# Kernel optimization log

Hardware: AMD Instinct MI355X
Metric: run time of the kernel (lower is better)

The kernel has to match this reference:

```python
import jax, jax.numpy as jnp
import numpy as np

EPS = 1e-5
K = 20  # n. neighbors


def _lrelu(x):
    return jnp.where(x >= 0, x, 0.2 * x)


def _bn(x, gamma, beta):
    # training-mode batchnorm over all axes except channel axis 1
    axes = tuple(i for i in range(x.ndim) if i != 1)
    m = jnp.mean(x, axis=axes, keepdims=True)
    v = jnp.var(x, axis=axes, keepdims=True)
    shape = [1, x.shape[1]] + [1] * (x.ndim - 2)
    return (x - m) * jax.lax.rsqrt(v + EPS) * gamma.reshape(shape) + beta.reshape(shape)


def _knn(x, k):
    # x: (B, C, N) -> idx (B, N, k) of nearest neighbors (largest negative sq dist)
    xx = jnp.sum(x * x, axis=1)                      # (B, N)
    inner = jnp.einsum('bcn,bcm->bnm', x, x)          # (B, N, N)
    dist = -xx[:, :, None] + 2.0 * inner - xx[:, None, :]
    _, idx = jax.lax.top_k(dist, k)
    return idx


def _graph_feature(x, k):
    # x: (B, C, N) -> edge features (B, 2C, N, k)
    B = x.shape[0]
    idx = _knn(x, k)                                  # (B, N, k)
    xt = jnp.transpose(x, (0, 2, 1))                  # (B, N, C)
    nbr = xt[jnp.arange(B)[:, None, None], idx]       # (B, N, k, C)
    ctr = xt[:, :, None, :]                           # (B, N, 1, C)
    edge = jnp.concatenate([nbr - ctr, jnp.broadcast_to(ctr, nbr.shape)], axis=-1)
    return jnp.transpose(edge, (0, 3, 1, 2))          # (B, 2C, N, k)


def _conv1d(W, x):
    return jnp.einsum('oc,bcn->bon', W, x)


def _conv2d(W, x):
    return jnp.einsum('oc,bcnk->bonk', W, x)


def setup_inputs() -> dict:
    key = jax.random.key(0)
    ks = jax.random.split(key, 10)
    w = lambda k, s: jax.random.normal(k, s, jnp.float32) * 0.05
    d = {
        'x': jax.random.normal(ks[0], (4, 3, 4096), jnp.float32),
        'W1': w(ks[1], (64, 3)),
        'W2': w(ks[2], (64, 128)),
        'W3': w(ks[3], (64, 128)),
        'W4': w(ks[4], (512, 64)),
        'W5': w(ks[5], (512, 704)),
        'W6': w(ks[6], (256, 512)),
        'W7': w(ks[7], (128, 256)),
        'W8': w(ks[8], (2, 128)),
        'bias8': jnp.zeros((2,), jnp.float32),
    }
    bn_ch = [64, 64, 64, 512, 512, 256, 128]
    for i, c in enumerate(bn_ch, start=1):
        d[f'gamma{i}'] = jnp.ones((c,), jnp.float32)
        d[f'beta{i}'] = jnp.zeros((c,), jnp.float32)
    return d


def reference(x, W1, W2, W3, W4, W5, W6, W7, W8, bias8,
              gamma1, beta1, gamma2, beta2, gamma3, beta3, gamma4, beta4,
              gamma5, beta5, gamma6, beta6, gamma7, beta7):
    N = x.shape[2]
    x1 = _lrelu(_bn(_conv1d(W1, x), gamma1, beta1))                 # (B,64,N)
    e2 = _graph_feature(x1, K)                                      # (B,128,N,k)
    x2 = _lrelu(_bn(_conv2d(W2, e2), gamma2, beta2)).max(axis=-1)   # (B,64,N)
    e3 = _graph_feature(x2, K)
    x3 = _lrelu(_bn(_conv2d(W3, e3), gamma3, beta3)).max(axis=-1)   # (B,64,N)
    x6 = _lrelu(_bn(_conv1d(W4, x3), gamma4, beta4))                # (B,512,N)
    x6 = jnp.broadcast_to(x6.max(axis=-1, keepdims=True), (x6.shape[0], x6.shape[1], N))
    x7 = jnp.concatenate([x1, x2, x3, x6], axis=1)                  # (B,704,N)
    x7 = _lrelu(_bn(_conv1d(W5, x7), gamma5, beta5))
    x7 = _lrelu(_bn(_conv1d(W6, x7), gamma6, beta6))
    x7 = _lrelu(_bn(_conv1d(W7, x7), gamma7, beta7))
    return _conv1d(W8, x7) + bias8[None, :, None]                   # (B,2,N)
```

## Files before the change

kernel.cpp:

```cpp
#include <hip/hip_runtime.h>
#include <math.h>

#define NN 4096
#define BB 4
#define NPT (NN*BB)
#define KK 20
#define EPSB 1e-5f

#define AS_STRIDE 132
#define WS_STRIDE 68
#define SKEW(c) ((((((c)>>2)&7))<<2) + (((c)>>5)*28))

__device__ __forceinline__ float lrelu(float x){ return x >= 0.f ? x : 0.2f*x; }

__device__ __forceinline__ unsigned fkey(float x){
  unsigned u = __float_as_uint(x);
  return u ^ (unsigned)(((int)u >> 31) | 0x80000000);
}

__global__ void conv1_kernel(const float* __restrict__ x, const float* __restrict__ W1,
                             float* __restrict__ xcat){
  __shared__ float Wl[192];
  int tid = threadIdx.x;
  if (tid < 192) Wl[tid] = W1[tid];
  __syncthreads();
  int p = blockIdx.x*4 + (tid >> 6);
  int o = tid & 63;
  int b = p >> 12, n = p & 4095;
  const float* xb = x + (size_t)b*3*NN + n;
  float acc = Wl[o*3+0]*xb[0] + Wl[o*3+1]*xb[NN] + Wl[o*3+2]*xb[2*NN];
  xcat[(size_t)p*192 + o] = acc;
}

__global__ void stats_pm_kernel(const float* __restrict__ buf, int stride, int ofs,
                                float* __restrict__ psum, float* __restrict__ psumsq, int C){
  int tid = threadIdx.x;
  int lane = tid & 63, g = tid >> 6;
  int o = blockIdx.x*64 + lane;
  int p0 = blockIdx.y*256 + g*64;
  float s = 0.f, ss = 0.f;
  for (int i = 0; i < 64; ++i){
    float v = buf[(size_t)(p0+i)*stride + ofs + o];
    s += v; ss += v*v;
  }
  __shared__ float rs[4][64], rss[4][64];
  rs[g][lane] = s; rss[g][lane] = ss;
  __syncthreads();
  if (g == 0){
    s  = rs[0][lane]+rs[1][lane]+rs[2][lane]+rs[3][lane];
    ss = rss[0][lane]+rss[1][lane]+rss[2][lane]+rss[3][lane];
    psum[(size_t)blockIdx.y*C + o] = s;
    psumsq[(size_t)blockIdx.y*C + o] = ss;
  }
}

__global__ void bn_finalize_kernel(const float* __restrict__ psum, const float* __restrict__ psumsq,
                                   int nparts,
                                   const float* __restrict__ gamma, const float* __restrict__ beta,
                                   float* __restrict__ scale, float* __restrict__ shift,
                                   float invcnt, int C){
  int o = threadIdx.x + blockIdx.x*blockDim.x;
  if (o >= C) return;
  float s = 0.f, ss = 0.f;
  for (int i = 0; i < nparts; ++i){
    s  += psum[(size_t)i*C + o];
    ss += psumsq[(size_t)i*C + o];
  }
  float m = s*invcnt;
  float v = ss*invcnt - m*m;
  v = fmaxf(v, 0.f);
  float sc = gamma[o] * rsqrtf(v + EPSB);
  scale[o] = sc;
  shift[o] = beta[o] - m*sc;
}

__global__ void apply_bn_kernel(float* __restrict__ buf, int stride, int ofs, int log2C,
                                const float* __restrict__ scale, const float* __restrict__ shift){
  int i = blockIdx.x*256 + threadIdx.x;
  int o = i & ((1<<log2C)-1);
  int p = i >> log2C;
  size_t a = (size_t)p*stride + ofs + o;
  float e = buf[a]*scale[o] + shift[o];
  buf[a] = lrelu(e);
}

__global__ void xx_kernel(const float* __restrict__ xcat, int stride, int ofs,
                          float* __restrict__ xx){
  int p = blockIdx.x*256 + threadIdx.x;
  const float4* r = (const float4*)(xcat + (size_t)p*stride + ofs);
  float s = 0.f;
  #pragma unroll
  for (int i = 0; i < 16; ++i){ float4 v = r[i]; s += v.x*v.x + v.y*v.y + v.z*v.z + v.w*v.w; }
  xx[p] = s;
}

__global__ void __launch_bounds__(256, 2)
dist_kernel(const float* __restrict__ xcat, int ofs,
            const float* __restrict__ xx, float* __restrict__ dist,
            unsigned* __restrict__ gmaxp, int b){
  int bx = blockIdx.x, by = blockIdx.y;
  if (by > bx) return;
  __shared__ float As[32*AS_STRIDE + 64];
  __shared__ float Bs[32*AS_STRIDE + 64];
  int tid = threadIdx.x;
  int n0 = by*128, m0 = bx*128;
  const float* base = xcat + (size_t)b*NN*192 + ofs;
  int pA = (tid >> 4)*4, oB = (tid & 15)*4;
  int cgrp = (tid & 7)*4;
  float acc[8][8] = {};
  for (int h = 0; h < 2; ++h){
    int cb = h*32;
    float4 vin[4], vw[4];
    #pragma unroll
    for (int j = 0; j < 4; ++j){
      int row = (tid + 256*j) >> 3;
      vin[j] = *(const float4*)(base + (size_t)(n0+row)*192 + cb + cgrp);
      vw[j]  = *(const float4*)(base + (size_t)(m0+row)*192 + cb + cgrp);
    }
    if (h) __syncthreads();
    #pragma unroll
    for (int j = 0; j < 4; ++j){
      int row = (tid + 256*j) >> 3, c4 = cgrp;
      float4 v = vin[j];
      As[(c4+0)*AS_STRIDE+SKEW(c4+0)+row]=v.x; As[(c4+1)*AS_STRIDE+SKEW(c4+1)+row]=v.y;
      As[(c4+2)*AS_STRIDE+SKEW(c4+2)+row]=v.z; As[(c4+3)*AS_STRIDE+SKEW(c4+3)+row]=v.w;
      float4 w = vw[j];
      Bs[(c4+0)*AS_STRIDE+SKEW(c4+0)+row]=w.x; Bs[(c4+1)*AS_STRIDE+SKEW(c4+1)+row]=w.y;
      Bs[(c4+2)*AS_STRIDE+SKEW(c4+2)+row]=w.z; Bs[(c4+3)*AS_STRIDE+SKEW(c4+3)+row]=w.w;
    }
    __syncthreads();
    for (int c = 0; c < 32; ++c){
      const float* arow = &As[c*AS_STRIDE + SKEW(c)];
      const float* brow = &Bs[c*AS_STRIDE + SKEW(c)];
      float4 a0 = *(const float4*)&arow[pA];
      float4 a1 = *(const float4*)&arow[pA + 64];
      float4 b0 = *(const float4*)&brow[oB];
      float4 b1 = *(const float4*)&brow[oB + 64];
      float av[8] = {a0.x,a0.y,a0.z,a0.w,a1.x,a1.y,a1.z,a1.w};
      float bv[8] = {b0.x,b0.y,b0.z,b0.w,b1.x,b1.y,b1.z,b1.w};
      #pragma unroll
      for (int i = 0; i < 8; ++i)
        #pragma unroll
        for (int j = 0; j < 8; ++j)
          acc[i][j] += av[i]*bv[j];
    }
  }
  float xmv[8], xnv[8];
  #pragma unroll
  for (int j = 0; j < 4; ++j){
    xmv[j]   = xx[b*NN + m0 + oB + j];
    xmv[4+j] = xx[b*NN + m0 + 64 + oB + j];
    xnv[j]   = xx[b*NN + n0 + pA + j];
    xnv[4+j] = xx[b*NN + n0 + 64 + pA + j];
  }
  #pragma unroll
  for (int h = 0; h < 2; ++h){
    #pragma unroll
    for (int i = 0; i < 4; ++i){
      int row = n0 + h*64 + pA + i;
      float xn = xnv[h*4 + i];
      int ai = h*4 + i;
      float4 w0, w1;
      w0.x = 2.f*acc[ai][0] - xn - xmv[0]; w0.y = 2.f*acc[ai][1] - xn - xmv[1];
      w0.z = 2.f*acc[ai][2] - xn - xmv[2]; w0.w = 2.f*acc[ai][3] - xn - xmv[3];
      w1.x = 2.f*acc[ai][4] - xn - xmv[4]; w1.y = 2.f*acc[ai][5] - xn - xmv[5];
      w1.z = 2.f*acc[ai][6] - xn - xmv[6]; w1.w = 2.f*acc[ai][7] - xn - xmv[7];
      float* drow = dist + (size_t)row*NN + m0;
      *(float4*)(drow + oB) = w0;
      *(float4*)(drow + 64 + oB) = w1;
      unsigned gm = fkey(w0.x), t;
      t = fkey(w0.y); if (t > gm) gm = t;
      t = fkey(w0.z); if (t > gm) gm = t;
      t = fkey(w0.w); if (t > gm) gm = t;
      t = fkey(w1.x); if (t > gm) gm = t;
      t = fkey(w1.y); if (t > gm) gm = t;
      t = fkey(w1.z); if (t > gm) gm = t;
      t = fkey(w1.w); if (t > gm) gm = t;
      gmaxp[(size_t)row*512 + (bx<<4) + (oB>>2)] = gm;
    }
  }
  if (bx != by){
    #pragma unroll
    for (int jh = 0; jh < 2; ++jh){
      #pragma unroll
      for (int jj = 0; jj < 4; ++jj){
        int j = jh*4 + jj;
        float xm = xmv[j];
        float4 lo, hi;
        lo.x = 2.f*acc[0][j] - xm - xnv[0];
        lo.y = 2.f*acc[1][j] - xm - xnv[1];
        lo.z = 2.f*acc[2][j] - xm - xnv[2];
        lo.w = 2.f*acc[3][j] - xm - xnv[3];
        hi.x = 2.f*acc[4][j] - xm - xnv[4];
        hi.y = 2.f*acc[5][j] - xm - xnv[5];
        hi.z = 2.f*acc[6][j] - xm - xnv[6];
        hi.w = 2.f*acc[7][j] - xm - xnv[7];
        int mrow = m0 + jh*64 + oB + jj;
        float* drow = dist + (size_t)mrow*NN + n0;
        *(float4*)(drow + pA) = lo;
        *(float4*)(drow + 64 + pA) = hi;
        unsigned gm = fkey(lo.x), t;
        t = fkey(lo.y); if (t > gm) gm = t;
        t = fkey(lo.z); if (t > gm) gm = t;
        t = fkey(lo.w); if (t > gm) gm = t;
        t = fkey(hi.x); if (t > gm) gm = t;
        t = fkey(hi.y); if (t > gm) gm = t;
        t = fkey(hi.z); if (t > gm) gm = t;
        t = fkey(hi.w); if (t > gm) gm = t;
        gmaxp[(size_t)mrow*512 + (by<<4) + (pA>>2)] = gm;
      }
    }
  }
}

__global__ void __launch_bounds__(256)
topk_kernel(const float* __restrict__ dist, const unsigned* __restrict__ gmax,
            int* __restrict__ idxout){
  __shared__ unsigned lv[4][256], li[4][256];
  __shared__ unsigned lcnt[4];
  int wv = threadIdx.x >> 6, lane = threadIdx.x & 63;
  int n = blockIdx.x*4 + wv;
  const unsigned* grow = gmax + (size_t)n*512;
  unsigned g[8];
  #pragma unroll
  for (int j = 0; j < 8; ++j) g[j] = grow[j*64 + lane];
  if (lane == 0) lcnt[wv] = 0u;
  unsigned prefix = 0u, act = 0xFFu; int need = KK; int tot = 512;
  for (int b = 31; b >= 16; --b){
    unsigned m = 0u;
    #pragma unroll
    for (int j = 0; j < 8; ++j) m |= ((g[j] >> b) & 1u) << j;
    unsigned c = (unsigned)__popc(m & act);
    #pragma unroll
    for (int s = 1; s < 64; s <<= 1) c += __shfl_xor(c, s);
    if ((int)c >= need){ act &= m; prefix |= (1u << b); tot = (int)c; }
    else { need -= (int)c; act &= ~m; tot -= (int)c; }
    if (KK - need + tot <= 44) break;
  }
  unsigned T = prefix;
  const float* drow = dist + (size_t)n*NN;
  #pragma unroll
  for (int j = 0; j < 8; ++j){
    if (g[j] >= T){
      int gid = j*64 + lane;
      int cbase = ((gid >> 4) << 7) + ((gid & 15) << 2);
      float4 v0 = *(const float4*)(drow + cbase);
      float4 v1 = *(const float4*)(drow + cbase + 64);
      unsigned k0=fkey(v0.x),k1=fkey(v0.y),k2=fkey(v0.z),k3=fkey(v0.w);
      unsigned k4=fkey(v1.x),k5=fkey(v1.y),k6=fkey(v1.z),k7=fkey(v1.w);
      int q = (k0>=T)+(k1>=T)+(k2>=T)+(k3>=T)+(k4>=T)+(k5>=T)+(k6>=T)+(k7>=T);
      unsigned pos = atomicAdd(&lcnt[wv], (unsigned)q);
      #define PUTC(kx,cofs) if (kx >= T){ if (pos < 256u){ lv[wv][pos]=kx; li[wv][pos]=(unsigned)(cbase+(cofs)); } pos++; }
      PUTC(k0,0) PUTC(k1,1) PUTC(k2,2) PUTC(k3,3)
      PUTC(k4,64) PUTC(k5,65) PUTC(k6,66) PUTC(k7,67)
      #undef PUTC
    }
  }
  unsigned C = lcnt[wv];
  int* orow = idxout + (size_t)n*KK;
  if (C <= 64u){
    unsigned kv = 0u, ki = 0xFFFFFFFFu;
    if (lane < (int)C){ kv = lv[wv][lane]; ki = li[wv][lane]; }
    #pragma unroll
    for (int k = 2; k <= 64; k <<= 1){
      #pragma unroll
      for (int j2 = k >> 1; j2 > 0; j2 >>= 1){
        unsigned ov = __shfl_xor(kv, j2);
        unsigned oi = __shfl_xor(ki, j2);
        bool iLower = ((lane & j2) == 0);
        bool dirDesc = ((lane & k) == 0);
        bool mineGr = (kv > ov) || (kv == ov && ki < oi);
        bool keep = dirDesc ? (iLower ? mineGr : !mineGr)
                            : (iLower ? !mineGr : mineGr);
        kv = keep ? kv : ov;
        ki = keep ? ki : oi;
      }
    }
    if (lane < KK) orow[lane] = (int)ki;
  } else {
    unsigned rv[KK], ri[KK];
    #pragma unroll
    for (int q = 0; q < KK; ++q){ rv[q]=0u; ri[q]=0xFFFFFFFFu; }
    #pragma unroll
    for (int j = 0; j < 8; ++j){
      if (g[j] >= T){
        int gid = j*64 + lane;
        int cbase = ((gid >> 4) << 7) + ((gid & 15) << 2);
        float4 v0 = *(const float4*)(drow + cbase);
        float4 v1 = *(const float4*)(drow + cbase + 64);
        float f0[8] = {v0.x,v0.y,v0.z,v0.w,v1.x,v1.y,v1.z,v1.w};
        #pragma unroll
        for (int t = 0; t < 8; ++t){
          unsigned u = fkey(f0[t]);
          unsigned ix = (unsigned)(cbase + ((t < 4) ? t : (60 + t)));
          bool beat = (u > rv[KK-1]) || (u == rv[KK-1] && ix < ri[KK-1]);
          if (u >= T && beat){
            unsigned pv = u, pi = ix;
            #pragma unroll
            for (int p = 0; p < KK; ++p){
              bool keep2 = (rv[p] > pv) || (rv[p] == pv && ri[p] < pi);
              unsigned nv = keep2 ? rv[p] : pv;
              unsigned ni = keep2 ? ri[p] : pi;
              pv = keep2 ? pv : rv[p];
              pi = keep2 ? pi : ri[p];
              rv[p] = nv; ri[p] = ni;
            }
          }
        }
      }
    }
    for (int q = 0; q < KK; ++q){
      unsigned bv = rv[0], bi = ri[0];
      #pragma unroll
      for (int s = 1; s < 64; s <<= 1){
        unsigned ov = __shfl_xor(bv, s);
        unsigned oi = __shfl_xor(bi, s);
        bool take = (ov > bv) || (ov == bv && oi < bi);
        bv = take ? ov : bv;
        bi = take ? oi : bi;
      }
      if (rv[0] == bv && ri[0] == bi){
        #pragma unroll
        for (int p = 0; p < KK-1; ++p){ rv[p] = rv[p+1]; ri[p] = ri[p+1]; }
        rv[KK-1] = 0u; ri[KK-1] = 0xFFFFFFFFu;
      }
      if (lane == 0) orow[q] = (int)bi;
    }
  }
}

__global__ void ut_kernel(const float* __restrict__ xcat, int ofs, const float* __restrict__ W,
                          float* __restrict__ U, float* __restrict__ T){
  __shared__ float Wl[64*129];
  int tid = threadIdx.x;
  for (int i = tid; i < 64*128; i += 256){
    int o = i >> 7, c = i & 127;
    Wl[o*129 + c] = W[i];
  }
  __syncthreads();
  int g = tid >> 6, lane = tid & 63;
  int p = blockIdx.x*4 + g;
  float xv = xcat[(size_t)p*192 + ofs + lane];
  const float* wr = Wl + lane*129;
  float u = 0.f, t = 0.f;
  for (int c = 0; c < 64; ++c){
    float xc = __shfl(xv, c);
    float wa = wr[c], wb = wr[64+c];
    u += wa*xc;
    t += (wb - wa)*xc;
  }
  U[(size_t)p*64 + lane] = u;
  T[(size_t)p*64 + lane] = t;
}

__global__ void gather_kernel(const float* __restrict__ U, const float* __restrict__ T,
                              const int* __restrict__ idx,
                              float* __restrict__ psum, float* __restrict__ psumsq,
                              float* __restrict__ vmax, float* __restrict__ vmin){
  int tid = threadIdx.x;
  int g = tid >> 6, lane = tid & 63;
  int p0 = blockIdx.x*64 + g*16;
  float s = 0.f, ss = 0.f;
  for (int pi = 0; pi < 16; ++pi){
    int p = p0 + pi;
    int base = (p >> 12) << 12;
    float t = T[(size_t)p*64 + lane];
    const int* ir = idx + (size_t)p*KK;
    float mx = -INFINITY, mn = INFINITY;
    for (int k = 0; k < KK; ++k){
      int j = ir[k];
      float v = U[(size_t)(base + j)*64 + lane] + t;
      s += v; ss += v*v;
      mx = fmaxf(mx, v); mn = fminf(mn, v);
    }
    vmax[(size_t)p*64 + lane] = mx;
    vmin[(size_t)p*64 + lane] = mn;
  }
  __shared__ float rs[4][64], rss[4][64];
  rs[g][lane] = s; rss[g][lane] = ss;
  __syncthreads();
  if (g == 0){
    s  = rs[0][lane]+rs[1][lane]+rs[2][lane]+rs[3][lane];
    ss = rss[0][lane]+rss[1][lane]+rss[2][lane]+rss[3][lane];
    psum[(size_t)blockIdx.x*64 + lane] = s;
    psumsq[(size_t)blockIdx.x*64 + lane] = ss;
  }
}

__global__ void gapply_kernel(const float* __restrict__ vmax, const float* __restrict__ vmin,
                              const float* __restrict__ scale, const float* __restrict__ shift,
                              float* __restrict__ xcat, int ofs){
  int i = blockIdx.x*256 + threadIdx.x;
  int p = i >> 6, o = i & 63;
  float s = scale[o];
  float v = (s >= 0.f) ? vmax[i] : vmin[i];
  xcat[(size_t)p*192 + ofs + o] = lrelu(s*v + shift[o]);
}

__global__ void __launch_bounds__(256, 2)
mm_kernel(const float* __restrict__ in, int inStride, int inOfs,
          const float* __restrict__ W, int wStride,
          float* __restrict__ out, int outStride,
          const float* __restrict__ bias, int O, int I,
          const float* __restrict__ bnScale, const float* __restrict__ bnShift){
  __shared__ float As[32*AS_STRIDE + 64];
  __shared__ float Ws[32*WS_STRIDE + 64];
  int tid = threadIdx.x;
  int p0 = blockIdx.x*128, o0 = blockIdx.y*64;
  int psub = (tid >> 4)*8, osub = (tid & 15)*4;
  int cgrp = (tid & 7)*4;
  float acc[8][4] = {};
  for (int cc = 0; cc < I; cc += 32){
    float4 sc4 = make_float4(1.f,1.f,1.f,1.f), sh4 = make_float4(0.f,0.f,0.f,0.f);
    if (bnScale){
      sc4 = *(const float4*)(bnScale + cc + cgrp);
      sh4 = *(const float4*)(bnShift + cc + cgrp);
    }
    float4 vin[4], vw[2];
    #pragma unroll
    for (int j = 0; j < 4; ++j){
      int row = (tid + 256*j) >> 3;
      vin[j] = *(const float4*)(in + (size_t)(p0+row)*inStride + inOfs + cc + cgrp);
    }
    #pragma unroll
    for (int j = 0; j < 2; ++j){
      int row = (tid + 256*j) >> 3;
      vw[j] = *(const float4*)(W + (size_t)(o0+row)*wStride + cc + cgrp);
    }
    if (cc) __syncthreads();
    #pragma unroll
    for (int j = 0; j < 4; ++j){
      int row = (tid + 256*j) >> 3, c4 = cgrp;
      float4 v = vin[j];
      if (bnScale){
        v.x = lrelu(v.x*sc4.x + sh4.x); v.y = lrelu(v.y*sc4.y + sh4.y);
        v.z = lrelu(v.z*sc4.z + sh4.z); v.w = lrelu(v.w*sc4.w + sh4.w);
      }
      As[(c4+0)*AS_STRIDE+SKEW(c4+0)+row]=v.x; As[(c4+1)*AS_STRIDE+SKEW(c4+1)+row]=v.y;
      As[(c4+2)*AS_STRIDE+SKEW(c4+2)+row]=v.z; As[(c4+3)*AS_STRIDE+SKEW(c4+3)+row]=v.w;
    }
    #pragma unroll
    for (int j = 0; j < 2; ++j){
      int row = (tid + 256*j) >> 3, c4 = cgrp;
      float4 v = vw[j];
      Ws[(c4+0)*WS_STRIDE+SKEW(c4+0)+row]=v.x; Ws[(c4+1)*WS_STRIDE+SKEW(c4+1)+row]=v.y;
      Ws[(c4+2)*WS_STRIDE+SKEW(c4+2)+row]=v.z; Ws[(c4+3)*WS_STRIDE+SKEW(c4+3)+row]=v.w;
    }
    __syncthreads();
    for (int c = 0; c < 32; ++c){
      const float* arow = &As[c*AS_STRIDE + SKEW(c)];
      const float* brow = &Ws[c*WS_STRIDE + SKEW(c)];
      float4 a0 = *(const float4*)&arow[psub];
      float4 a1 = *(const float4*)&arow[psub + 4];
      float4 bb = *(const float4*)&brow[osub];
      float av[8] = {a0.x,a0.y,a0.z,a0.w,a1.x,a1.y,a1.z,a1.w};
      float bv[4] = {bb.x,bb.y,bb.z,bb.w};
      #pragma unroll
      for (int i = 0; i < 8; ++i)
        #pragma unroll
        for (int j = 0; j < 4; ++j)
          acc[i][j] += av[i]*bv[j];
    }
  }
  int bIdx = p0 >> 12;
  float bb0=0.f, bb1=0.f, bb2=0.f, bb3=0.f;
  if (bias){
    bb0 = bias[bIdx*O + o0 + osub + 0];
    bb1 = bias[bIdx*O + o0 + osub + 1];
    bb2 = bias[bIdx*O + o0 + osub + 2];
    bb3 = bias[bIdx*O + o0 + osub + 3];
  }
  #pragma unroll
  for (int i = 0; i < 8; ++i){
    float4 w;
    w.x = acc[i][0]+bb0; w.y = acc[i][1]+bb1; w.z = acc[i][2]+bb2; w.w = acc[i][3]+bb3;
    *(float4*)(out + (size_t)(p0+psub+i)*outStride + o0 + osub) = w;
  }
}

__global__ void __launch_bounds__(256, 2)
mm64_kernel(const float* __restrict__ in, int inStride, int inOfs,
            const float* __restrict__ W, int wStride,
            float* __restrict__ out, int outStride,
            int O, int I,
            const float* __restrict__ bnScale, const float* __restrict__ bnShift){
  __shared__ float As[32*WS_STRIDE + 64];
  __shared__ float Ws[32*WS_STRIDE + 64];
  int tid = threadIdx.x;
  int p0 = blockIdx.x*64, o0 = blockIdx.y*64;
  int psub = (tid >> 4)*4, osub = (tid & 15)*4;
  int cgrp = (tid & 7)*4;
  float acc[4][4] = {};
  for (int cc = 0; cc < I; cc += 32){
    float4 sc4 = make_float4(1.f,1.f,1.f,1.f), sh4 = make_float4(0.f,0.f,0.f,0.f);
    if (bnScale){
      sc4 = *(const float4*)(bnScale + cc + cgrp);
      sh4 = *(const float4*)(bnShift + cc + cgrp);
    }
    float4 vin[2], vw[2];
    #pragma unroll
    for (int j = 0; j < 2; ++j){
      int row = (tid + 256*j) >> 3;
      vin[j] = *(const float4*)(in + (size_t)(p0+row)*inStride + inOfs + cc + cgrp);
      vw[j]  = *(const float4*)(W + (size_t)(o0+row)*wStride + cc + cgrp);
    }
    if (cc) __syncthreads();
    #pragma unroll
    for (int j = 0; j < 2; ++j){
      int row = (tid + 256*j) >> 3, c4 = cgrp;
      float4 v = vin[j];
      if (bnScale){
        v.x = lrelu(v.x*sc4.x + sh4.x); v.y = lrelu(v.y*sc4.y + sh4.y);
        v.z = lrelu(v.z*sc4.z + sh4.z); v.w = lrelu(v.w*sc4.w + sh4.w);
      }
      As[(c4+0)*WS_STRIDE+SKEW(c4+0)+row]=v.x; As[(c4+1)*WS_STRIDE+SKEW(c4+1)+row]=v.y;
      As[(c4+2)*WS_STRIDE+SKEW(c4+2)+row]=v.z; As[(c4+3)*WS_STRIDE+SKEW(c4+3)+row]=v.w;
      float4 w = vw[j];
      Ws[(c4+0)*WS_STRIDE+SKEW(c4+0)+row]=w.x; Ws[(c4+1)*WS_STRIDE+SKEW(c4+1)+row]=w.y;
      Ws[(c4+2)*WS_STRIDE+SKEW(c4+2)+row]=w.z; Ws[(c4+3)*WS_STRIDE+SKEW(c4+3)+row]=w.w;
    }
    __syncthreads();
    for (int c = 0; c < 32; ++c){
      const float* arow = &As[c*WS_STRIDE + SKEW(c)];
      const float* brow = &Ws[c*WS_STRIDE + SKEW(c)];
      float4 a0 = *(const float4*)&arow[psub];
      float4 bb = *(const float4*)&brow[osub];
      float av[4] = {a0.x,a0.y,a0.z,a0.w};
      float bv[4] = {bb.x,bb.y,bb.z,bb.w};
      #pragma unroll
      for (int i = 0; i < 4; ++i)
        #pragma unroll
        for (int j = 0; j < 4; ++j)
          acc[i][j] += av[i]*bv[j];
    }
  }
  #pragma unroll
  for (int i = 0; i < 4; ++i){
    float4 w;
    w.x = acc[i][0]; w.y = acc[i][1]; w.z = acc[i][2]; w.w = acc[i][3];
    *(float4*)(out + (size_t)(p0+psub+i)*outStride + o0 + osub) = w;
  }
}

__global__ void __launch_bounds__(256, 2)
conv4stats_kernel(const float* __restrict__ xcat, const float* __restrict__ W4,
                  float* __restrict__ psum, float* __restrict__ psumsq,
                  float* __restrict__ pmax, float* __restrict__ pmin){
  __shared__ float As[32*AS_STRIDE + 64];
  __shared__ float Ws[32*AS_STRIDE + 64];
  int tid = threadIdx.x;
  int p0 = blockIdx.x*128, o0 = blockIdx.y*128;
  int pA = (tid >> 4)*4, oB = (tid & 15)*4;
  int cgrp = (tid & 7)*4;
  float acc[8][8] = {};
  for (int h = 0; h < 2; ++h){
    int cb = h*32;
    float4 vin[4], vw[4];
    #pragma unroll
    for (int j = 0; j < 4; ++j){
      int row = (tid + 256*j) >> 3;
      vin[j] = *(const float4*)(xcat + (size_t)(p0+row)*192 + 128 + cb + cgrp);
      vw[j]  = *(const float4*)(W4 + (size_t)(o0+row)*64 + cb + cgrp);
    }
    if (h) __syncthreads();
    #pragma unroll
    for (int j = 0; j < 4; ++j){
      int row = (tid + 256*j) >> 3, c4 = cgrp;
      float4 v = vin[j];
      As[(c4+0)*AS_STRIDE+SKEW(c4+0)+row]=v.x; As[(c4+1)*AS_STRIDE+SKEW(c4+1)+row]=v.y;
      As[(c4+2)*AS_STRIDE+SKEW(c4+2)+row]=v.z; As[(c4+3)*AS_STRIDE+SKEW(c4+3)+row]=v.w;
      float4 w = vw[j];
      Ws[(c4+0)*AS_STRIDE+SKEW(c4+0)+row]=w.x; Ws[(c4+1)*AS_STRIDE+SKEW(c4+1)+row]=w.y;
      Ws[(c4+2)*AS_STRIDE+SKEW(c4+2)+row]=w.z; Ws[(c4+3)*AS_STRIDE+SKEW(c4+3)+row]=w.w;
    }
    __syncthreads();
    for (int c = 0; c < 32; ++c){
      const float* arow = &As[c*AS_STRIDE + SKEW(c)];
      const float* brow = &Ws[c*AS_STRIDE + SKEW(c)];
      float4 a0 = *(const float4*)&arow[pA];
      float4 a1 = *(const float4*)&arow[pA + 64];
      float4 b0 = *(const float4*)&brow[oB];
      float4 b1 = *(const float4*)&brow[oB + 64];
      float av[8] = {a0.x,a0.y,a0.z,a0.w,a1.x,a1.y,a1.z,a1.w};
      float bv[8] = {b0.x,b0.y,b0.z,b0.w,b1.x,b1.y,b1.z,b1.w};
      #pragma unroll
      for (int i = 0; i < 8; ++i)
        #pragma unroll
        for (int j = 0; j < 8; ++j)
          acc[i][j] += av[i]*bv[j];
    }
  }
  float cs[8], cq[8], cmx[8], cmn[8];
  #pragma unroll
  for (int j = 0; j < 8; ++j){
    float s = 0.f, q = 0.f, mx = -INFINITY, mn = INFINITY;
    #pragma unroll
    for (int i = 0; i < 8; ++i){
      float v = acc[i][j];
      s += v; q += v*v; mx = fmaxf(mx, v); mn = fminf(mn, v);
    }
    cs[j]=s; cq[j]=q; cmx[j]=mx; cmn[j]=mn;
  }
  __syncthreads();
  int r = tid >> 4;
  #pragma unroll
  for (int j = 0; j < 8; ++j){
    int col = (j < 4) ? (oB + j) : (64 + oB + (j-4));
    As[r*128 + col]        = cs[j];
    As[2048 + r*128 + col] = cq[j];
    Ws[r*128 + col]        = cmx[j];
    Ws[2048 + r*128 + col] = cmn[j];
  }
  __syncthreads();
  if (tid < 128){
    float ts = 0.f, tq = 0.f, tm = -INFINITY, tn = INFINITY;
    for (int rr = 0; rr < 16; ++rr){
      ts += As[rr*128 + tid];
      tq += As[2048 + rr*128 + tid];
      tm = fmaxf(tm, Ws[rr*128 + tid]);
      tn = fminf(tn, Ws[2048 + rr*128 + tid]);
    }
    size_t slot = (size_t)blockIdx.x*512 + o0 + tid;
    psum[slot] = ts; psumsq[slot] = tq; pmax[slot] = tm; pmin[slot] = tn;
  }
}

__global__ void x6v_kernel(const float* __restrict__ pmax, const float* __restrict__ pmin,
                           const float* __restrict__ scale, const float* __restrict__ shift,
                           float* __restrict__ x6v){
  int t = blockIdx.x*256 + threadIdx.x;
  int b = t >> 9, o = t & 511;
  float mx = -INFINITY, mn = INFINITY;
  for (int pt = b*32; pt < b*32+32; ++pt){
    mx = fmaxf(mx, pmax[(size_t)pt*512 + o]);
    mn = fminf(mn, pmin[(size_t)pt*512 + o]);
  }
  float s = scale[o];
  float v = (s >= 0.f) ? mx : mn;
  x6v[t] = lrelu(s*v + shift[o]);
}

__global__ void bias5_kernel(const float* __restrict__ W5, const float* __restrict__ x6v,
                             float* __restrict__ b5){
  __shared__ float xl[512];
  int tid = threadIdx.x;
  int t = blockIdx.x*256 + tid;
  int b = t >> 9, o = t & 511;
  for (int i = tid; i < 512; i += 256) xl[i] = x6v[(b<<9) + i];
  __syncthreads();
  const float* wr = W5 + (size_t)o*704 + 192;
  float acc = 0.f;
  for (int c = 0; c < 512; ++c) acc += wr[c]*xl[c];
  b5[t] = acc;
}

__global__ void conv8_kernel(const float* __restrict__ r7, const float* __restrict__ W8,
                             const float* __restrict__ bias8,
                             const float* __restrict__ scale, const float* __restrict__ shift,
                             float* __restrict__ out){
  __shared__ float Wl[256];
  __shared__ float scl[128], shl[128];
  int tid = threadIdx.x;
  Wl[tid] = W8[tid];
  if (tid < 128){ scl[tid] = scale[tid]; shl[tid] = shift[tid]; }
  __syncthreads();
  int p = blockIdx.x*256 + tid;
  int b = p >> 12, n = p & 4095;
  const float4* row = (const float4*)(r7 + (size_t)p*128);
  float a0 = 0.f, a1 = 0.f;
  #pragma unroll
  for (int i = 0; i < 32; ++i){
    float4 v = row[i];
    v.x = lrelu(v.x*scl[i*4+0] + shl[i*4+0]);
    v.y = lrelu(v.y*scl[i*4+1] + shl[i*4+1]);
    v.z = lrelu(v.z*scl[i*4+2] + shl[i*4+2]);
    v.w = lrelu(v.w*scl[i*4+3] + shl[i*4+3]);
    a0 += v.x*Wl[i*4] + v.y*Wl[i*4+1] + v.z*Wl[i*4+2] + v.w*Wl[i*4+3];
    a1 += v.x*Wl[128+i*4] + v.y*Wl[128+i*4+1] + v.z*Wl[128+i*4+2] + v.w*Wl[128+i*4+3];
  }
  out[(size_t)(b*2+0)*NN + n] = a0 + bias8[0];
  out[(size_t)(b*2+1)*NN + n] = a1 + bias8[1];
}

extern "C" void kernel_launch(void* const* d_in, const int* in_sizes, int n_in,
                              void* d_out, int out_size, void* d_ws, size_t ws_size,
                              hipStream_t stream){
  const float* x     = (const float*)d_in[0];
  const float* W1    = (const float*)d_in[1];
  const float* W2    = (const float*)d_in[2];
  const float* W3    = (const float*)d_in[3];
  const float* W4    = (const float*)d_in[4];
  const float* W5    = (const float*)d_in[5];
  const float* W6    = (const float*)d_in[6];
  const float* W7    = (const float*)d_in[7];
  const float* W8    = (const float*)d_in[8];
  const float* bias8 = (const float*)d_in[9];
  const float* gamma[8]; const float* beta[8];
  for (int i = 1; i <= 7; ++i){
    gamma[i] = (const float*)d_in[10 + 2*(i-1)];
    beta[i]  = (const float*)d_in[11 + 2*(i-1)];
  }
  float* out = (float*)d_out;

  float* ws = (float*)d_ws;
  size_t off = 0;
  float* xcat  = ws + off; off += (size_t)NPT*192;
  float* U     = ws + off; off += (size_t)NPT*64;
  float* T     = ws + off; off += (size_t)NPT*64;
  float* xx    = ws + off; off += NPT;
  int*   idx   = (int*)(ws + off); off += (size_t)NPT*KK;
  float* psum  = ws + off; off += 128*512;
  float* psumsq= ws + off; off += 128*512;
  float* pmax  = ws + off; off += 128*512;
  float* pmin  = ws + off; off += 128*512;
  float* scale = ws + off; off += 512;
  float* shift = ws + off; off += 512;
  float* x6v   = ws + off; off += 2048;
  float* b5    = ws + off; off += 2048;
  float* big   = ws + off;
  float* dist  = big;
  float* vmaxB = big;
  float* vminB = big + (size_t)NPT*64;
  float* r5    = big;
  float* r6    = big + (size_t)NPT*512;
  float* r7    = big + (size_t)NPT*512 + (size_t)NPT*256;
  unsigned* gmaxU = (unsigned*)U;

  conv1_kernel<<<NPT/4, 256, 0, stream>>>(x, W1, xcat);
  stats_pm_kernel<<<dim3(1,64), 256, 0, stream>>>(xcat, 192, 0, psum, psumsq, 64);
  bn_finalize_kernel<<<1, 64, 0, stream>>>(psum, psumsq, 64, gamma[1], beta[1], scale, shift, 1.f/16384.f, 64);
  apply_bn_kernel<<<NPT*64/256, 256, 0, stream>>>(xcat, 192, 0, 6, scale, shift);

  xx_kernel<<<NPT/256, 256, 0, stream>>>(xcat, 192, 0, xx);
  for (int b = 0; b < BB; ++b){
    dist_kernel<<<dim3(32,32), 256, 0, stream>>>(xcat, 0, xx, dist, gmaxU, b);
    topk_kernel<<<NN/4, 256, 0, stream>>>(dist, gmaxU, idx + (size_t)b*NN*KK);
  }

  ut_kernel<<<NPT/4, 256, 0, stream>>>(xcat, 0, W2, U, T);
  gather_kernel<<<256, 256, 0, stream>>>(U, T, idx, psum, psumsq, vmaxB, vminB);
  bn_finalize_kernel<<<1, 64, 0, stream>>>(psum, psumsq, 256, gamma[2], beta[2], scale, shift, 1.f/327680.f, 64);
  gapply_kernel<<<NPT*64/256, 256, 0, stream>>>(vmaxB, vminB, scale, shift, xcat, 64);

  xx_kernel<<<NPT/256, 256, 0, stream>>>(xcat, 192, 64, xx);
  for (int b = 0; b < BB; ++b){
    dist_kernel<<<dim3(32,32), 256, 0, stream>>>(xcat, 64, xx, dist, gmaxU, b);
    topk_kernel<<<NN/4, 256, 0, stream>>>(dist, gmaxU, idx + (size_t)b*NN*KK);
  }

  ut_kernel<<<NPT/4, 256, 0, stream>>>(xcat, 64, W3, U, T);
  gather_kernel<<<256, 256, 0, stream>>>(U, T, idx, psum, psumsq, vmaxB, vminB);
  bn_finalize_kernel<<<1, 64, 0, stream>>>(psum, psumsq, 256, gamma[3], beta[3], scale, shift, 1.f/327680.f, 64);
  gapply_kernel<<<NPT*64/256, 256, 0, stream>>>(vmaxB, vminB, scale, shift, xcat, 128);

  conv4stats_kernel<<<dim3(NPT/128, 4), 256, 0, stream>>>(xcat, W4, psum, psumsq, pmax, pmin);
  bn_finalize_kernel<<<1, 512, 0, stream>>>(psum, psumsq, 128, gamma[4], beta[4], scale, shift, 1.f/16384.f, 512);
  x6v_kernel<<<8, 256, 0, stream>>>(pmax, pmin, scale, shift, x6v);
  bias5_kernel<<<8, 256, 0, stream>>>(W5, x6v, b5);

  mm_kernel<<<dim3(NPT/128, 8), 256, 0, stream>>>(xcat, 192, 0, W5, 704, r5, 512, b5, 512, 192, nullptr, nullptr);
  stats_pm_kernel<<<dim3(8,64), 256, 0, stream>>>(r5, 512, 0, psum, psumsq, 512);
  bn_finalize_kernel<<<1, 512, 0, stream>>>(psum, psumsq, 64, gamma[5], beta[5], scale, shift, 1.f/16384.f, 512);

  mm64_kernel<<<dim3(NPT/64, 4), 256, 0, stream>>>(r5, 512, 0, W6, 512, r6, 256, 256, 512, scale, shift);
  stats_pm_kernel<<<dim3(4,64), 256, 0, stream>>>(r6, 256, 0, psum, psumsq, 256);
  bn_finalize_kernel<<<1, 256, 0, stream>>>(psum, psumsq, 64, gamma[6], beta[6], scale, shift, 1.f/16384.f, 256);

  mm64_kernel<<<dim3(NPT/64, 2), 256, 0, stream>>>(r6, 256, 0, W7, 256, r7, 128, 128, 256, scale, shift);
  stats_pm_kernel<<<dim3(2,64), 256, 0, stream>>>(r7, 128, 0, psum, psumsq, 128);
  bn_finalize_kernel<<<1, 128, 0, stream>>>(psum, psumsq, 64, gamma[7], beta[7], scale, shift, 1.f/16384.f, 128);

  conv8_kernel<<<NPT/256, 256, 0, stream>>>(r7, W8, bias8, scale, shift, out);
}
```

Measured before the change: 1.090 ms.

## Batch kNN distance and top-k over all batches; amortize ut_kernel weight load

The dist and topk kernels now take a z grid dimension over the batch, so all four batches run in one launch each when the workspace is large enough, falling back to the per-batch loop otherwise. This is meant to cut launch count and fill the GPU better, since each per-batch dist launch only runs about 528 useful blocks. In exchange it needs a 4x larger distance buffer, which means more memory footprint and less L2 reuse between dist and topk. Separately, ut_kernel now has each block handle 16 points instead of 4, spreading the shared-memory weight load over more work.

```diff
diff --git a/kernel.cpp b/kernel.cpp
--- a/kernel.cpp
+++ b/kernel.cpp
@@ -97,12 +97,15 @@
 __global__ void __launch_bounds__(256, 2)
 dist_kernel(const float* __restrict__ xcat, int ofs,
             const float* __restrict__ xx, float* __restrict__ dist,
-            unsigned* __restrict__ gmaxp, int b){
+            unsigned* __restrict__ gmaxp, int b0){
   int bx = blockIdx.x, by = blockIdx.y;
   if (by > bx) return;
   __shared__ float As[32*AS_STRIDE + 64];
   __shared__ float Bs[32*AS_STRIDE + 64];
   int tid = threadIdx.x;
+  int b = b0 + blockIdx.z;
+  float* distb = dist + (size_t)blockIdx.z*NN*NN;
+  unsigned* gmaxb = gmaxp + (size_t)blockIdx.z*NN*512;
   int n0 = by*128, m0 = bx*128;
   const float* base = xcat + (size_t)b*NN*192 + ofs;
   int pA = (tid >> 4)*4, oB = (tid & 15)*4;
@@ -134,10 +137,10 @@
       const float* brow = &Bs[c*AS_STRIDE + SKEW(c)];
       float4 a0 = *(const float4*)&arow[pA];
       float4 a1 = *(const float4*)&arow[pA + 64];
-      float4 b0 = *(const float4*)&brow[oB];
-      float4 b1 = *(const float4*)&brow[oB + 64];
+      float4 b0v = *(const float4*)&brow[oB];
+      float4 b1v = *(const float4*)&brow[oB + 64];
       float av[8] = {a0.x,a0.y,a0.z,a0.w,a1.x,a1.y,a1.z,a1.w};
-      float bv[8] = {b0.x,b0.y,b0.z,b0.w,b1.x,b1.y,b1.z,b1.w};
+      float bv[8] = {b0v.x,b0v.y,b0v.z,b0v.w,b1v.x,b1v.y,b1v.z,b1v.w};
       #pragma unroll
       for (int i = 0; i < 8; ++i)
         #pragma unroll
@@ -165,7 +168,7 @@
       w0.z = 2.f*acc[ai][2] - xn - xmv[2]; w0.w = 2.f*acc[ai][3] - xn - xmv[3];
       w1.x = 2.f*acc[ai][4] - xn - xmv[4]; w1.y = 2.f*acc[ai][5] - xn - xmv[5];
       w1.z = 2.f*acc[ai][6] - xn - xmv[6]; w1.w = 2.f*acc[ai][7] - xn - xmv[7];
-      float* drow = dist + (size_t)row*NN + m0;
+      float* drow = distb + (size_t)row*NN + m0;
       *(float4*)(drow + oB) = w0;
       *(float4*)(drow + 64 + oB) = w1;
       unsigned gm = fkey(w0.x), t;
@@ -176,7 +179,7 @@
       t = fkey(w1.y); if (t > gm) gm = t;
       t = fkey(w1.z); if (t > gm) gm = t;
       t = fkey(w1.w); if (t > gm) gm = t;
-      gmaxp[(size_t)row*512 + (bx<<4) + (oB>>2)] = gm;
+      gmaxb[(size_t)row*512 + (bx<<4) + (oB>>2)] = gm;
     }
   }
   if (bx != by){
@@ -196,7 +199,7 @@
         hi.z = 2.f*acc[6][j] - xm - xnv[6];
         hi.w = 2.f*acc[7][j] - xm - xnv[7];
         int mrow = m0 + jh*64 + oB + jj;
-        float* drow = dist + (size_t)mrow*NN + n0;
+        float* drow = distb + (size_t)mrow*NN + n0;
         *(float4*)(drow + pA) = lo;
         *(float4*)(drow + 64 + pA) = hi;
         unsigned gm = fkey(lo.x), t;
@@ -207,7 +210,7 @@
         t = fkey(hi.y); if (t > gm) gm = t;
         t = fkey(hi.z); if (t > gm) gm = t;
         t = fkey(hi.w); if (t > gm) gm = t;
-        gmaxp[(size_t)mrow*512 + (by<<4) + (pA>>2)] = gm;
+        gmaxb[(size_t)mrow*512 + (by<<4) + (pA>>2)] = gm;
       }
     }
   }
@@ -220,7 +223,10 @@
   __shared__ unsigned lcnt[4];
   int wv = threadIdx.x >> 6, lane = threadIdx.x & 63;
   int n = blockIdx.x*4 + wv;
-  const unsigned* grow = gmax + (size_t)n*512;
+  const float* distb = dist + (size_t)blockIdx.z*NN*NN;
+  const unsigned* gmaxb = gmax + (size_t)blockIdx.z*NN*512;
+  int* idxb = idxout + (size_t)blockIdx.z*NN*KK;
+  const unsigned* grow = gmaxb + (size_t)n*512;
   unsigned g[8];
   #pragma unroll
   for (int j = 0; j < 8; ++j) g[j] = grow[j*64 + lane];
@@ -238,7 +244,7 @@
     if (KK - need + tot <= 44) break;
   }
   unsigned T = prefix;
-  const float* drow = dist + (size_t)n*NN;
+  const float* drow = distb + (size_t)n*NN;
   #pragma unroll
   for (int j = 0; j < 8; ++j){
     if (g[j] >= T){
@@ -257,7 +263,7 @@
     }
   }
   unsigned C = lcnt[wv];
-  int* orow = idxout + (size_t)n*KK;
+  int* orow = idxb + (size_t)n*KK;
   if (C <= 64u){
     unsigned kv = 0u, ki = 0xFFFFFFFFu;
     if (lane < (int)C){ kv = lv[wv][lane]; ki = li[wv][lane]; }
@@ -339,18 +345,21 @@
   }
   __syncthreads();
   int g = tid >> 6, lane = tid & 63;
-  int p = blockIdx.x*4 + g;
-  float xv = xcat[(size_t)p*192 + ofs + lane];
   const float* wr = Wl + lane*129;
-  float u = 0.f, t = 0.f;
-  for (int c = 0; c < 64; ++c){
-    float xc = __shfl(xv, c);
-    float wa = wr[c], wb = wr[64+c];
-    u += wa*xc;
-    t += (wb - wa)*xc;
-  }
-  U[(size_t)p*64 + lane] = u;
-  T[(size_t)p*64 + lane] = t;
+  #pragma unroll
+  for (int q = 0; q < 4; ++q){
+    int p = blockIdx.x*16 + g*4 + q;
+    float xv = xcat[(size_t)p*192 + ofs + lane];
+    float u = 0.f, t = 0.f;
+    for (int c = 0; c < 64; ++c){
+      float xc = __shfl(xv, c);
+      float wa = wr[c], wb = wr[64+c];
+      u += wa*xc;
+      t += (wb - wa)*xc;
+    }
+    U[(size_t)p*64 + lane] = u;
+    T[(size_t)p*64 + lane] = t;
+  }
 }
 
 __global__ void gather_kernel(const float* __restrict__ U, const float* __restrict__ T,
@@ -726,29 +735,44 @@
   float* r7    = big + (size_t)NPT*512 + (size_t)NPT*256;
   unsigned* gmaxU = (unsigned*)U;
 
+  size_t bigBatched = (size_t)4*NN*NN + (size_t)4*NN*512;
+  bool knnBatched = ws_size >= (off + bigBatched) * sizeof(float);
+  float* dist4 = big;
+  unsigned* gmax4 = (unsigned*)(big + (size_t)4*NN*NN);
+
   conv1_kernel<<<NPT/4, 256, 0, stream>>>(x, W1, xcat);
   stats_pm_kernel<<<dim3(1,64), 256, 0, stream>>>(xcat, 192, 0, psum, psumsq, 64);
   bn_finalize_kernel<<<1, 64, 0, stream>>>(psum, psumsq, 64, gamma[1], beta[1], scale, shift, 1.f/16384.f, 64);
   apply_bn_kernel<<<NPT*64/256, 256, 0, stream>>>(xcat, 192, 0, 6, scale, shift);
 
   xx_kernel<<<NPT/256, 256, 0, stream>>>(xcat, 192, 0, xx);
-  for (int b = 0; b < BB; ++b){
-    dist_kernel<<<dim3(32,32), 256, 0, stream>>>(xcat, 0, xx, dist, gmaxU, b);
-    topk_kernel<<<NN/4, 256, 0, stream>>>(dist, gmaxU, idx + (size_t)b*NN*KK);
-  }
-
-  ut_kernel<<<NPT/4, 256, 0, stream>>>(xcat, 0, W2, U, T);
+  if (knnBatched){
+    dist_kernel<<<dim3(32,32,BB), 256, 0, stream>>>(xcat, 0, xx, dist4, gmax4, 0);
+    topk_kernel<<<dim3(NN/4,1,BB), 256, 0, stream>>>(dist4, gmax4, idx);
+  } else {
+    for (int b = 0; b < BB; ++b){
+      dist_kernel<<<dim3(32,32,1), 256, 0, stream>>>(xcat, 0, xx, dist, gmaxU, b);
+      topk_kernel<<<dim3(NN/4,1,1), 256, 0, stream>>>(dist, gmaxU, idx + (size_t)b*NN*KK);
+    }
+  }
+
+  ut_kernel<<<NPT/16, 256, 0, stream>>>(xcat, 0, W2, U, T);
   gather_kernel<<<256, 256, 0, stream>>>(U, T, idx, psum, psumsq, vmaxB, vminB);
   bn_finalize_kernel<<<1, 64, 0, stream>>>(psum, psumsq, 256, gamma[2], beta[2], scale, shift, 1.f/327680.f, 64);
   gapply_kernel<<<NPT*64/256, 256, 0, stream>>>(vmaxB, vminB, scale, shift, xcat, 64);
 
   xx_kernel<<<NPT/256, 256, 0, stream>>>(xcat, 192, 64, xx);
-  for (int b = 0; b < BB; ++b){
-    dist_kernel<<<dim3(32,32), 256, 0, stream>>>(xcat, 64, xx, dist, gmaxU, b);
-    topk_kernel<<<NN/4, 256, 0, stream>>>(dist, gmaxU, idx + (size_t)b*NN*KK);
-  }
-
-  ut_kernel<<<NPT/4, 256, 0, stream>>>(xcat, 64, W3, U, T);
+  if (knnBatched){
+    dist_kernel<<<dim3(32,32,BB), 256, 0, stream>>>(xcat, 64, xx, dist4, gmax4, 0);
+    topk_kernel<<<dim3(NN/4,1,BB), 256, 0, stream>>>(dist4, gmax4, idx);
+  } else {
+    for (int b = 0; b < BB; ++b){
+      dist_kernel<<<dim3(32,32,1), 256, 0, stream>>>(xcat, 64, xx, dist, gmaxU, b);
+      topk_kernel<<<dim3(NN/4,1,1), 256, 0, stream>>>(dist, gmaxU, idx + (size_t)b*NN*KK);
+    }
+  }
+
+  ut_kernel<<<NPT/16, 256, 0, stream>>>(xcat, 64, W3, U, T);
   gather_kernel<<<256, 256, 0, stream>>>(U, T, idx, psum, psumsq, vmaxB, vminB);
   bn_finalize_kernel<<<1, 64, 0, stream>>>(psum, psumsq, 256, gamma[3], beta[3], scale, shift, 1.f/327680.f, 64);
   gapply_kernel<<<NPT*64/256, 256, 0, stream>>>(vmaxB, vminB, scale, shift, xcat, 128);
```

Result: slower. 1.444 ms (+32.5%).
